# Optimization experiments

Measured on AMD Instinct MI355X. Metric: run time of the kernel, lower is better.

Reference implementation:

```python
import jax, jax.numpy as jnp
import numpy as np

DIM_HEAD = 64
REL_POS_DIM_HEAD = 32
SCALE = DIM_HEAD ** (-0.5)
REL_POS_SCALE = REL_POS_DIM_HEAD ** (-0.5)


def setup_inputs() -> dict:
    key = jax.random.key(0)
    k1, k2, k3, k4, k5 = jax.random.split(key, 5)
    B, H, S = 2, 16, 2048
    keys = jax.random.normal(k1, (B, H, S, DIM_HEAD), dtype=jnp.float32)
    queries = jax.random.normal(k2, (B, H, S, DIM_HEAD), dtype=jnp.float32)
    pos_key = jax.random.normal(k3, (B, H, S, REL_POS_DIM_HEAD), dtype=jnp.float32)
    pos_query = jax.random.normal(k4, (B, H, S, REL_POS_DIM_HEAD), dtype=jnp.float32)
    mask = jax.random.randint(k5, (B, S), 0, 2).astype(jnp.bool_)
    return {"keys": keys, "queries": queries, "pos_key": pos_key,
            "pos_query": pos_query, "mask": mask}


def reference(keys, queries, pos_key, pos_query, mask) -> jnp.ndarray:
    # clamp inputs to [-5, 5] as in the original module
    k = jnp.clip(keys, -5.0, 5.0)
    q = jnp.clip(queries, -5.0, 5.0)
    # content scores: [B, H, Q, K]
    dots = jnp.einsum("bhqd,bhkd->bhqk", q, k) * SCALE
    # relative-position scores
    pk = jnp.clip(pos_key, -5.0, 5.0)
    pq = jnp.clip(pos_query, -5.0, 5.0)
    dots = dots + jnp.einsum("bhqd,bhkd->bhqk", pq, pk) * REL_POS_SCALE
    # mask: True keys are not attended to; broadcast (B, K) -> (B, 1, 1, K)
    dots = jnp.where(mask[:, None, None, :], -jnp.inf, dots)
    return jax.nn.softmax(dots, axis=-1)
```

## Files before the change

### kernel.cpp

```cpp
#include <hip/hip_runtime.h>
#include <cstdint>
#include <cstddef>

#define SEQ 2048
#define TILES 16
#define FRAG_SHORTS 12288
#define FRAG_BYTES  24576
#define PSTRIDE 68

typedef __attribute__((ext_vector_type(8))) short bf16x8;
typedef __attribute__((ext_vector_type(4))) float f32x4;
typedef __attribute__((ext_vector_type(4))) short short4v;
typedef __attribute__((ext_vector_type(2))) unsigned uint2v;

__device__ __forceinline__ short f2bf(float f) {
    union { float f; unsigned u; } a; a.f = f;
    unsigned r = a.u + 0x7fffu + ((a.u >> 16) & 1u);
    return (short)(r >> 16);
}
__device__ __forceinline__ float clip5(float v) { return fminf(fmaxf(v, -5.0f), 5.0f); }
__device__ __forceinline__ float bflo2f(unsigned u) { union { unsigned u; float f; } a; a.u = u << 16; return a.f; }
__device__ __forceinline__ float bfhi2f(unsigned u) { union { unsigned u; float f; } a; a.u = u & 0xffff0000u; return a.f; }

__global__ __launch_bounds__(256)
void prep_kernel(const float* __restrict__ Kp, const float* __restrict__ PKp,
                 short* __restrict__ wsK)
{
    int id = blockIdx.x * 256 + threadIdx.x;
    int q = id % 24;
    int row = id / 24;
    int bh = row >> 11;
    int col = row & 2047;
    int tile = col >> 7;
    int st = (col >> 4) & 7;
    int l15 = col & 15;
    float4 v;
    int f, dd;
    if (q < 16) {
        v = reinterpret_cast<const float4*>(Kp)[(size_t)row * 16 + q];
        f = q >> 3;
        dd = (q & 7) * 4;
    } else {
        v = reinterpret_cast<const float4*>(PKp)[(size_t)row * 8 + (q - 16)];
        f = 2;
        dd = (q - 16) * 4;
    }
    int ll = l15 | ((dd >> 3) << 4);
    int j = dd & 7;
    short4v s4;
    s4[0] = f2bf(clip5(v.x)); s4[1] = f2bf(clip5(v.y));
    s4[2] = f2bf(clip5(v.z)); s4[3] = f2bf(clip5(v.w));
    *reinterpret_cast<short4v*>(wsK + ((size_t)bh * TILES + tile) * FRAG_SHORTS
                                + (((st * 3 + f) * 64 + ll) << 3) + j) = s4;
}

template<bool USEWS>
__global__ __launch_bounds__(512, 4)
void attn_map_kernel(const float* __restrict__ Kp, const float* __restrict__ Qp,
                     const float* __restrict__ PKp, const float* __restrict__ PQp,
                     const int* __restrict__ maskp, const short* __restrict__ wsK,
                     float* __restrict__ out)
{
    __shared__ short lds_k[2][FRAG_SHORTS];
    __shared__ float lds_madd[SEQ];
    __shared__ short lds_p[8 * 16 * PSTRIDE];
    __shared__ float lds_inv[128];

    const int p = blockIdx.x;
    const int x = p & 7;
    const int slot = p >> 3;
    const int bh = x + 8 * (slot >> 4);
    const int qg = slot & 15;

    const int tid = threadIdx.x;
    const int lane = tid & 63;
    const int w = tid >> 6;
    const int l15 = lane & 15;
    const int l4 = lane >> 4;

    const int qrow = qg * 128 + w * 16 + l15;

    const float* Qb  = Qp  + (size_t)bh * (SEQ * 64);
    const float* PQb = PQp + (size_t)bh * (SEQ * 32);
    const int*   mb  = maskp + (size_t)(bh >> 4) * SEQ;
    float* outb = out + (size_t)bh * SEQ * SEQ;

    const float QS  = 0.125f * 1.4426950408889634f;
    const float PQS = 0.17677669529663687f * 1.4426950408889634f;
    const float SHIFT = 28.853900817779268f;

    bf16x8 qa[3];
    #pragma unroll
    for (int f = 0; f < 2; ++f) {
        const float* src = Qb + (size_t)qrow * 64 + f * 32 + l4 * 8;
        bf16x8 v;
        #pragma unroll
        for (int j = 0; j < 8; ++j) v[j] = f2bf(clip5(src[j]) * QS);
        qa[f] = v;
    }
    {
        const float* src = PQb + (size_t)qrow * 32 + l4 * 8;
        bf16x8 v;
        #pragma unroll
        for (int j = 0; j < 8; ++j) v[j] = f2bf(clip5(src[j]) * PQS);
        qa[2] = v;
    }

    #pragma unroll
    for (int i = 0; i < SEQ / 512; ++i) {
        int idx = i * 512 + tid;
        lds_madd[idx] = (mb[idx] ? -1e30f : 0.0f) - SHIFT;
    }

    const short* kf = USEWS ? (wsK + (size_t)bh * (TILES * FRAG_SHORTS)) : nullptr;

#define STAGE(T, B) do {                                                                   \
    if constexpr (USEWS) {                                                                 \
        const char* ksrc = (const char*)kf + (size_t)(T) * FRAG_BYTES;                     \
        _Pragma("unroll")                                                                  \
        for (int c = 0; c < 3; ++c) {                                                      \
            int off = w * 3072 + c * 1024;                                                 \
            __builtin_amdgcn_global_load_lds(                                              \
                (const __attribute__((address_space(1))) void*)(ksrc + off + lane * 16),   \
                (__attribute__((address_space(3))) void*)((char*)&lds_k[(B)][0] + off),    \
                16, 0, 0);                                                                 \
        }                                                                                  \
    } else {                                                                               \
        const int tile0 = (T) * 128;                                                       \
        _Pragma("unroll")                                                                  \
        for (int i = 0; i < 6; ++i) {                                                      \
            int e = i * 512 + tid;                                                         \
            int col = e / 24, dq = e - col * 24, d0 = dq * 4;                               \
            int colg = tile0 + col;                                                        \
            float4 v; int f, dd;                                                           \
            if (d0 < 64) {                                                                 \
                v = *reinterpret_cast<const float4*>(Kp + (size_t)bh * (SEQ * 64) + (size_t)colg * 64 + d0); \
                f = d0 >> 5; dd = d0 & 31;                                                 \
            } else {                                                                       \
                v = *reinterpret_cast<const float4*>(PKp + (size_t)bh * (SEQ * 32) + (size_t)colg * 32 + (d0 - 64)); \
                f = 2; dd = d0 - 64;                                                       \
            }                                                                              \
            int ll = (col & 15) | ((dd >> 3) << 4);                                        \
            int st2 = col >> 4, j = dd & 7;                                                \
            short4v s4;                                                                    \
            s4[0] = f2bf(clip5(v.x)); s4[1] = f2bf(clip5(v.y));                            \
            s4[2] = f2bf(clip5(v.z)); s4[3] = f2bf(clip5(v.w));                            \
            *reinterpret_cast<short4v*>(&lds_k[(B)][(((st2 * 3 + f) * 64 + ll) << 3) + j]) = s4; \
        }                                                                                  \
    }                                                                                      \
} while (0)

    float ssum = 0.0f;

    STAGE(0, 0);
    __syncthreads();

    #pragma unroll 1
    for (int t = 0; t < TILES; ++t) {
        STAGE((t + 1) & 15, (t + 1) & 1);
        const short* lk = &lds_k[t & 1][0];
        #pragma unroll
        for (int st = 0; st < 8; ++st) {
            bf16x8 kb0 = *reinterpret_cast<const bf16x8*>(lk + ((st * 3 + 0) * 64 + lane) * 8);
            bf16x8 kb1 = *reinterpret_cast<const bf16x8*>(lk + ((st * 3 + 1) * 64 + lane) * 8);
            bf16x8 kb2 = *reinterpret_cast<const bf16x8*>(lk + ((st * 3 + 2) * 64 + lane) * 8);
            f32x4 madd4 = *reinterpret_cast<const f32x4*>(&lds_madd[t * 128 + st * 16 + l4 * 4]);
            f32x4 acc = {0.f, 0.f, 0.f, 0.f};
            acc = __builtin_amdgcn_mfma_f32_16x16x32_bf16(kb0, qa[0], acc, 0, 0, 0);
            acc = __builtin_amdgcn_mfma_f32_16x16x32_bf16(kb1, qa[1], acc, 0, 0, 0);
            acc = __builtin_amdgcn_mfma_f32_16x16x32_bf16(kb2, qa[2], acc, 0, 0, 0);
            float e0 = exp2f(acc[0] + madd4[0]);
            float e1 = exp2f(acc[1] + madd4[1]);
            float e2 = exp2f(acc[2] + madd4[2]);
            float e3 = exp2f(acc[3] + madd4[3]);
            ssum += (e0 + e1) + (e2 + e3);
        }
        __syncthreads();
    }

    {
        float s = ssum;
        s += __shfl_xor(s, 16);
        s += __shfl_xor(s, 32);
        if (lane < 16) lds_inv[w * 16 + l15] = 1.0f / s;
    }

    short* pw = &lds_p[w * (16 * PSTRIDE)];
    const int rowbase = qg * 128 + w * 16;

    #pragma unroll 1
    for (int t = 0; t < TILES; ++t) {
        if (t + 1 < TILES) STAGE(t + 1, (t + 1) & 1);
        const short* lk = &lds_k[t & 1][0];
        #pragma unroll
        for (int h = 0; h < 2; ++h) {
            #pragma unroll
            for (int sti = 0; sti < 4; ++sti) {
                const int st = h * 4 + sti;
                bf16x8 kb0 = *reinterpret_cast<const bf16x8*>(lk + ((st * 3 + 0) * 64 + lane) * 8);
                bf16x8 kb1 = *reinterpret_cast<const bf16x8*>(lk + ((st * 3 + 1) * 64 + lane) * 8);
                bf16x8 kb2 = *reinterpret_cast<const bf16x8*>(lk + ((st * 3 + 2) * 64 + lane) * 8);
                f32x4 madd4 = *reinterpret_cast<const f32x4*>(&lds_madd[t * 128 + st * 16 + l4 * 4]);
                f32x4 acc = {0.f, 0.f, 0.f, 0.f};
                acc = __builtin_amdgcn_mfma_f32_16x16x32_bf16(kb0, qa[0], acc, 0, 0, 0);
                acc = __builtin_amdgcn_mfma_f32_16x16x32_bf16(kb1, qa[1], acc, 0, 0, 0);
                acc = __builtin_amdgcn_mfma_f32_16x16x32_bf16(kb2, qa[2], acc, 0, 0, 0);
                float e0 = exp2f(acc[0] + madd4[0]);
                float e1 = exp2f(acc[1] + madd4[1]);
                float e2 = exp2f(acc[2] + madd4[2]);
                float e3 = exp2f(acc[3] + madd4[3]);
                unsigned u0, u1;
                asm("v_cvt_pk_bf16_f32 %0, %1, %2" : "=v"(u0) : "v"(e0), "v"(e1));
                asm("v_cvt_pk_bf16_f32 %0, %1, %2" : "=v"(u1) : "v"(e2), "v"(e3));
                uint2v uu; uu[0] = u0; uu[1] = u1;
                *reinterpret_cast<uint2v*>(&pw[l15 * PSTRIDE + sti * 16 + l4 * 4]) = uu;
            }
            #pragma unroll
            for (int s = 0; s < 4; ++s) {
                const int rl = s * 4 + (lane >> 4);
                uint2v uu = *reinterpret_cast<const uint2v*>(&pw[rl * PSTRIDE + l15 * 4]);
                const float invr = lds_inv[w * 16 + rl];
                f32x4 pv = { bflo2f(uu[0]) * invr, bfhi2f(uu[0]) * invr,
                             bflo2f(uu[1]) * invr, bfhi2f(uu[1]) * invr };
                __builtin_nontemporal_store(pv,
                    reinterpret_cast<f32x4*>(outb + (size_t)(rowbase + rl) * SEQ
                                             + t * 128 + h * 64 + l15 * 4));
            }
        }
        __syncthreads();
    }
#undef STAGE
}

extern "C" void kernel_launch(void* const* d_in, const int* in_sizes, int n_in,
                              void* d_out, int out_size, void* d_ws, size_t ws_size,
                              hipStream_t stream) {
    const float* keys      = (const float*)d_in[0];
    const float* queries   = (const float*)d_in[1];
    const float* pos_key   = (const float*)d_in[2];
    const float* pos_query = (const float*)d_in[3];
    const int*   mask      = (const int*)d_in[4];
    float* outp = (float*)d_out;

    const size_t need = (size_t)32 * TILES * FRAG_SHORTS * sizeof(short);
    if (ws_size >= need) {
        short* wsK = (short*)d_ws;
        prep_kernel<<<dim3(6144), dim3(256), 0, stream>>>(keys, pos_key, wsK);
        attn_map_kernel<true><<<dim3(512), dim3(512), 0, stream>>>(
            keys, queries, pos_key, pos_query, mask, wsK, outp);
    } else {
        attn_map_kernel<false><<<dim3(512), dim3(512), 0, stream>>>(
            keys, queries, pos_key, pos_query, mask, nullptr, outp);
    }
}
```

Before: 165.5 us.

## Split softmax row-sum pass and store pass into separate kernels

Splits the fused two-pass kernel into a sums kernel, which computes each query row's inverse softmax denominator into workspace, and a store kernel, which reads those values and writes the normalized output. The store kernel no longer carries the first pass, so its register and LDS footprint is smaller and the write-heavy phase runs on its own. This adds a kernel launch and a small global round-trip for the inverses, and recomputes the Q fragments and mask in both kernels. Output stores also switch from nontemporal to regular stores, which changes caching behaviour for the 512 MB output write.

After: 184.8 us. +11.7%, slower.

```diff
diff --git a/kernel.cpp b/kernel.cpp
--- a/kernel.cpp
+++ b/kernel.cpp
@@ -7,6 +7,8 @@
 #define FRAG_SHORTS 12288
 #define FRAG_BYTES  24576
 #define PSTRIDE 68
+#define WSK_SHORTS ((size_t)32 * TILES * FRAG_SHORTS)
+#define WSINV_FLOATS 65536
 
 typedef __attribute__((ext_vector_type(8))) short bf16x8;
 typedef __attribute__((ext_vector_type(4))) float f32x4;
@@ -21,6 +23,10 @@
 __device__ __forceinline__ float clip5(float v) { return fminf(fmaxf(v, -5.0f), 5.0f); }
 __device__ __forceinline__ float bflo2f(unsigned u) { union { unsigned u; float f; } a; a.u = u << 16; return a.f; }
 __device__ __forceinline__ float bfhi2f(unsigned u) { union { unsigned u; float f; } a; a.u = u & 0xffff0000u; return a.f; }
+
+#define QS_C  (0.125f * 1.4426950408889634f)
+#define PQS_C (0.17677669529663687f * 1.4426950408889634f)
+#define SHIFT_C 28.853900817779268f
 
 __global__ __launch_bounds__(256)
 void prep_kernel(const float* __restrict__ Kp, const float* __restrict__ PKp,
@@ -53,66 +59,6 @@
     *reinterpret_cast<short4v*>(wsK + ((size_t)bh * TILES + tile) * FRAG_SHORTS
                                 + (((st * 3 + f) * 64 + ll) << 3) + j) = s4;
 }
-
-template<bool USEWS>
-__global__ __launch_bounds__(512, 4)
-void attn_map_kernel(const float* __restrict__ Kp, const float* __restrict__ Qp,
-                     const float* __restrict__ PKp, const float* __restrict__ PQp,
-                     const int* __restrict__ maskp, const short* __restrict__ wsK,
-                     float* __restrict__ out)
-{
-    __shared__ short lds_k[2][FRAG_SHORTS];
-    __shared__ float lds_madd[SEQ];
-    __shared__ short lds_p[8 * 16 * PSTRIDE];
-    __shared__ float lds_inv[128];
-
-    const int p = blockIdx.x;
-    const int x = p & 7;
-    const int slot = p >> 3;
-    const int bh = x + 8 * (slot >> 4);
-    const int qg = slot & 15;
-
-    const int tid = threadIdx.x;
-    const int lane = tid & 63;
-    const int w = tid >> 6;
-    const int l15 = lane & 15;
-    const int l4 = lane >> 4;
-
-    const int qrow = qg * 128 + w * 16 + l15;
-
-    const float* Qb  = Qp  + (size_t)bh * (SEQ * 64);
-    const float* PQb = PQp + (size_t)bh * (SEQ * 32);
-    const int*   mb  = maskp + (size_t)(bh >> 4) * SEQ;
-    float* outb = out + (size_t)bh * SEQ * SEQ;
-
-    const float QS  = 0.125f * 1.4426950408889634f;
-    const float PQS = 0.17677669529663687f * 1.4426950408889634f;
-    const float SHIFT = 28.853900817779268f;
-
-    bf16x8 qa[3];
-    #pragma unroll
-    for (int f = 0; f < 2; ++f) {
-        const float* src = Qb + (size_t)qrow * 64 + f * 32 + l4 * 8;
-        bf16x8 v;
-        #pragma unroll
-        for (int j = 0; j < 8; ++j) v[j] = f2bf(clip5(src[j]) * QS);
-        qa[f] = v;
-    }
-    {
-        const float* src = PQb + (size_t)qrow * 32 + l4 * 8;
-        bf16x8 v;
-        #pragma unroll
-        for (int j = 0; j < 8; ++j) v[j] = f2bf(clip5(src[j]) * PQS);
-        qa[2] = v;
-    }
-
-    #pragma unroll
-    for (int i = 0; i < SEQ / 512; ++i) {
-        int idx = i * 512 + tid;
-        lds_madd[idx] = (mb[idx] ? -1e30f : 0.0f) - SHIFT;
-    }
-
-    const short* kf = USEWS ? (wsK + (size_t)bh * (TILES * FRAG_SHORTS)) : nullptr;
 
 #define STAGE(T, B) do {                                                                   \
     if constexpr (USEWS) {                                                                 \
@@ -150,14 +96,67 @@
     }                                                                                      \
 } while (0)
 
+#define PROLOGUE()                                                                          \
+    bf16x8 qa[3];                                                                           \
+    _Pragma("unroll")                                                                       \
+    for (int f = 0; f < 2; ++f) {                                                           \
+        const float* src = Qb + (size_t)qrow * 64 + f * 32 + l4 * 8;                        \
+        bf16x8 v;                                                                           \
+        _Pragma("unroll")                                                                   \
+        for (int j = 0; j < 8; ++j) v[j] = f2bf(clip5(src[j]) * QS_C);                      \
+        qa[f] = v;                                                                          \
+    }                                                                                       \
+    {                                                                                       \
+        const float* src = PQb + (size_t)qrow * 32 + l4 * 8;                                \
+        bf16x8 v;                                                                           \
+        _Pragma("unroll")                                                                   \
+        for (int j = 0; j < 8; ++j) v[j] = f2bf(clip5(src[j]) * PQS_C);                     \
+        qa[2] = v;                                                                          \
+    }                                                                                       \
+    _Pragma("unroll")                                                                       \
+    for (int i = 0; i < SEQ / 512; ++i) {                                                   \
+        int idx = i * 512 + tid;                                                            \
+        lds_madd[idx] = (mb[idx] ? -1e30f : 0.0f) - SHIFT_C;                                \
+    }
+
+template<bool USEWS>
+__global__ __launch_bounds__(512, 4)
+void sums_kernel(const float* __restrict__ Kp, const float* __restrict__ Qp,
+                 const float* __restrict__ PKp, const float* __restrict__ PQp,
+                 const int* __restrict__ maskp, const short* __restrict__ wsK,
+                 float* __restrict__ wsInv)
+{
+    __shared__ short lds_k[2][FRAG_SHORTS];
+    __shared__ float lds_madd[SEQ];
+
+    const int p = blockIdx.x;
+    const int x = p & 7;
+    const int slot = p >> 3;
+    const int bh = x + 8 * (slot >> 4);
+    const int qg = slot & 15;
+
+    const int tid = threadIdx.x;
+    const int lane = tid & 63;
+    const int w = tid >> 6;
+    const int l15 = lane & 15;
+    const int l4 = lane >> 4;
+    const int qrow = qg * 128 + w * 16 + l15;
+
+    const float* Qb  = Qp  + (size_t)bh * (SEQ * 64);
+    const float* PQb = PQp + (size_t)bh * (SEQ * 32);
+    const int*   mb  = maskp + (size_t)(bh >> 4) * SEQ;
+
+    PROLOGUE();
+
+    const short* kf = USEWS ? (wsK + (size_t)bh * (TILES * FRAG_SHORTS)) : nullptr;
+
     float ssum = 0.0f;
-
     STAGE(0, 0);
     __syncthreads();
 
     #pragma unroll 1
     for (int t = 0; t < TILES; ++t) {
-        STAGE((t + 1) & 15, (t + 1) & 1);
+        if (t + 1 < TILES) STAGE(t + 1, (t + 1) & 1);
         const short* lk = &lds_k[t & 1][0];
         #pragma unroll
         for (int st = 0; st < 8; ++st) {
@@ -178,7 +177,78 @@
         __syncthreads();
     }
 
-    {
+    float s = ssum;
+    s += __shfl_xor(s, 16);
+    s += __shfl_xor(s, 32);
+    if (lane < 16)
+        wsInv[(size_t)bh * SEQ + qrow] = 1.0f / s;
+}
+
+template<bool USEWS, bool HAVEINV>
+__global__ __launch_bounds__(512, 4)
+void store_kernel(const float* __restrict__ Kp, const float* __restrict__ Qp,
+                  const float* __restrict__ PKp, const float* __restrict__ PQp,
+                  const int* __restrict__ maskp, const short* __restrict__ wsK,
+                  const float* __restrict__ wsInv, float* __restrict__ out)
+{
+    __shared__ short lds_k[2][FRAG_SHORTS];
+    __shared__ float lds_madd[SEQ];
+    __shared__ short lds_p[8 * 16 * PSTRIDE];
+    __shared__ float lds_inv[128];
+
+    const int p = blockIdx.x;
+    const int x = p & 7;
+    const int slot = p >> 3;
+    const int bh = x + 8 * (slot >> 4);
+    const int qg = slot & 15;
+
+    const int tid = threadIdx.x;
+    const int lane = tid & 63;
+    const int w = tid >> 6;
+    const int l15 = lane & 15;
+    const int l4 = lane >> 4;
+    const int qrow = qg * 128 + w * 16 + l15;
+
+    const float* Qb  = Qp  + (size_t)bh * (SEQ * 64);
+    const float* PQb = PQp + (size_t)bh * (SEQ * 32);
+    const int*   mb  = maskp + (size_t)(bh >> 4) * SEQ;
+    float* outb = out + (size_t)bh * SEQ * SEQ;
+
+    PROLOGUE();
+
+    const short* kf = USEWS ? (wsK + (size_t)bh * (TILES * FRAG_SHORTS)) : nullptr;
+
+    STAGE(0, 0);
+
+    if constexpr (HAVEINV) {
+        if (lane < 16)
+            lds_inv[w * 16 + l15] = wsInv[(size_t)bh * SEQ + qrow];
+        __syncthreads();
+    } else {
+        __syncthreads();
+        float ssum = 0.0f;
+        #pragma unroll 1
+        for (int t = 0; t < TILES; ++t) {
+            STAGE((t + 1) & 15, (t + 1) & 1);
+            const short* lk = &lds_k[t & 1][0];
+            #pragma unroll
+            for (int st = 0; st < 8; ++st) {
+                bf16x8 kb0 = *reinterpret_cast<const bf16x8*>(lk + ((st * 3 + 0) * 64 + lane) * 8);
+                bf16x8 kb1 = *reinterpret_cast<const bf16x8*>(lk + ((st * 3 + 1) * 64 + lane) * 8);
+                bf16x8 kb2 = *reinterpret_cast<const bf16x8*>(lk + ((st * 3 + 2) * 64 + lane) * 8);
+                f32x4 madd4 = *reinterpret_cast<const f32x4*>(&lds_madd[t * 128 + st * 16 + l4 * 4]);
+                f32x4 acc = {0.f, 0.f, 0.f, 0.f};
+                acc = __builtin_amdgcn_mfma_f32_16x16x32_bf16(kb0, qa[0], acc, 0, 0, 0);
+                acc = __builtin_amdgcn_mfma_f32_16x16x32_bf16(kb1, qa[1], acc, 0, 0, 0);
+                acc = __builtin_amdgcn_mfma_f32_16x16x32_bf16(kb2, qa[2], acc, 0, 0, 0);
+                float e0 = exp2f(acc[0] + madd4[0]);
+                float e1 = exp2f(acc[1] + madd4[1]);
+                float e2 = exp2f(acc[2] + madd4[2]);
+                float e3 = exp2f(acc[3] + madd4[3]);
+                ssum += (e0 + e1) + (e2 + e3);
+            }
+            __syncthreads();
+        }
         float s = ssum;
         s += __shfl_xor(s, 16);
         s += __shfl_xor(s, 32);
@@ -222,14 +292,12 @@
                 const float invr = lds_inv[w * 16 + rl];
                 f32x4 pv = { bflo2f(uu[0]) * invr, bfhi2f(uu[0]) * invr,
                              bflo2f(uu[1]) * invr, bfhi2f(uu[1]) * invr };
-                __builtin_nontemporal_store(pv,
-                    reinterpret_cast<f32x4*>(outb + (size_t)(rowbase + rl) * SEQ
-                                             + t * 128 + h * 64 + l15 * 4));
+                *reinterpret_cast<f32x4*>(outb + (size_t)(rowbase + rl) * SEQ
+                                          + t * 128 + h * 64 + l15 * 4) = pv;
             }
         }
         __syncthreads();
     }
-#undef STAGE
 }
 
 extern "C" void kernel_launch(void* const* d_in, const int* in_sizes, int n_in,
@@ -242,14 +310,25 @@
     const int*   mask      = (const int*)d_in[4];
     float* outp = (float*)d_out;
 
-    const size_t need = (size_t)32 * TILES * FRAG_SHORTS * sizeof(short);
-    if (ws_size >= need) {
+    const size_t need_full = WSK_SHORTS * sizeof(short) + WSINV_FLOATS * sizeof(float);
+    const size_t need_inv  = WSINV_FLOATS * sizeof(float);
+
+    if (ws_size >= need_full) {
         short* wsK = (short*)d_ws;
+        float* wsInv = (float*)((char*)d_ws + WSK_SHORTS * sizeof(short));
         prep_kernel<<<dim3(6144), dim3(256), 0, stream>>>(keys, pos_key, wsK);
-        attn_map_kernel<true><<<dim3(512), dim3(512), 0, stream>>>(
-            keys, queries, pos_key, pos_query, mask, wsK, outp);
+        sums_kernel<true><<<dim3(512), dim3(512), 0, stream>>>(
+            keys, queries, pos_key, pos_query, mask, wsK, wsInv);
+        store_kernel<true, true><<<dim3(512), dim3(512), 0, stream>>>(
+            keys, queries, pos_key, pos_query, mask, wsK, wsInv, outp);
+    } else if (ws_size >= need_inv) {
+        float* wsInv = (float*)d_ws;
+        sums_kernel<false><<<dim3(512), dim3(512), 0, stream>>>(
+            keys, queries, pos_key, pos_query, mask, nullptr, wsInv);
+        store_kernel<false, true><<<dim3(512), dim3(512), 0, stream>>>(
+            keys, queries, pos_key, pos_query, mask, nullptr, wsInv, outp);
     } else {
-        attn_map_kernel<false><<<dim3(512), dim3(512), 0, stream>>>(
-            keys, queries, pos_key, pos_query, mask, nullptr, outp);
-    }
-}
+        store_kernel<false, false><<<dim3(512), dim3(512), 0, stream>>>(
+            keys, queries, pos_key, pos_query, mask, nullptr, nullptr, outp);
+    }
+}
```

## Cache exp values in registers to skip recompute; split blocks across column slices

Applied to the files above, without the earlier changes.

Each block now handles 32 query rows instead of 128. The 8 waves split into 2 row groups × 4 column slices, and the grid grows fourfold. The first pass stores the packed bf16 exponentials in a 64-entry register array. The second pass only normalizes and writes them out, with no second K staging and no MFMA recompute. Row sums are reduced across waves through shared memory. The risk is much higher VGPR pressure, which may cut occupancy or spill, and K is reloaded by four times as many blocks.

Result: faster. 149.4 us (median of 2 runs) (-9.7%).

```diff
diff --git a/kernel.cpp b/kernel.cpp
--- a/kernel.cpp
+++ b/kernel.cpp
@@ -6,7 +6,7 @@
 #define TILES 16
 #define FRAG_SHORTS 12288
 #define FRAG_BYTES  24576
-#define PSTRIDE 68
+#define PSTRIDE 36
 
 typedef __attribute__((ext_vector_type(8))) short bf16x8;
 typedef __attribute__((ext_vector_type(4))) float f32x4;
@@ -63,22 +63,25 @@
 {
     __shared__ short lds_k[2][FRAG_SHORTS];
     __shared__ float lds_madd[SEQ];
-    __shared__ short lds_p[8 * 16 * PSTRIDE];
-    __shared__ float lds_inv[128];
+    __shared__ short lds_p[8][16 * PSTRIDE];
+    __shared__ float sred[8][16];
+    __shared__ float lds_inv[8][16];
 
     const int p = blockIdx.x;
     const int x = p & 7;
     const int slot = p >> 3;
-    const int bh = x + 8 * (slot >> 4);
-    const int qg = slot & 15;
+    const int bh = x + 8 * (slot >> 6);
+    const int qb = slot & 63;
 
     const int tid = threadIdx.x;
     const int lane = tid & 63;
     const int w = tid >> 6;
     const int l15 = lane & 15;
     const int l4 = lane >> 4;
-
-    const int qrow = qg * 128 + w * 16 + l15;
+    const int rg = w & 1;
+    const int cs = w >> 1;
+
+    const int qrow = qb * 32 + rg * 16 + l15;
 
     const float* Qb  = Qp  + (size_t)bh * (SEQ * 64);
     const float* PQb = PQp + (size_t)bh * (SEQ * 32);
@@ -150,17 +153,19 @@
     }                                                                                      \
 } while (0)
 
+    unsigned pk[64];
     float ssum = 0.0f;
 
     STAGE(0, 0);
     __syncthreads();
 
-    #pragma unroll 1
+    #pragma unroll
     for (int t = 0; t < TILES; ++t) {
-        STAGE((t + 1) & 15, (t + 1) & 1);
+        if (t + 1 < TILES) STAGE(t + 1, (t + 1) & 1);
         const short* lk = &lds_k[t & 1][0];
         #pragma unroll
-        for (int st = 0; st < 8; ++st) {
+        for (int sti = 0; sti < 2; ++sti) {
+            const int st = cs * 2 + sti;
             bf16x8 kb0 = *reinterpret_cast<const bf16x8*>(lk + ((st * 3 + 0) * 64 + lane) * 8);
             bf16x8 kb1 = *reinterpret_cast<const bf16x8*>(lk + ((st * 3 + 1) * 64 + lane) * 8);
             bf16x8 kb2 = *reinterpret_cast<const bf16x8*>(lk + ((st * 3 + 2) * 64 + lane) * 8);
@@ -174,6 +179,11 @@
             float e2 = exp2f(acc[2] + madd4[2]);
             float e3 = exp2f(acc[3] + madd4[3]);
             ssum += (e0 + e1) + (e2 + e3);
+            unsigned u0, u1;
+            asm("v_cvt_pk_bf16_f32 %0, %1, %2" : "=v"(u0) : "v"(e0), "v"(e1));
+            asm("v_cvt_pk_bf16_f32 %0, %1, %2" : "=v"(u1) : "v"(e2), "v"(e3));
+            pk[t * 4 + sti * 2]     = u0;
+            pk[t * 4 + sti * 2 + 1] = u1;
         }
         __syncthreads();
     }
@@ -182,52 +192,41 @@
         float s = ssum;
         s += __shfl_xor(s, 16);
         s += __shfl_xor(s, 32);
-        if (lane < 16) lds_inv[w * 16 + l15] = 1.0f / s;
-    }
-
-    short* pw = &lds_p[w * (16 * PSTRIDE)];
-    const int rowbase = qg * 128 + w * 16;
-
-    #pragma unroll 1
+        if (lane < 16) sred[w][l15] = s;
+    }
+    __syncthreads();
+    {
+        const float rs = (sred[rg][l15] + sred[rg + 2][l15])
+                       + (sred[rg + 4][l15] + sred[rg + 6][l15]);
+        if (lane < 16) lds_inv[w][l15] = 1.0f / rs;
+    }
+
+    short* pw = &lds_p[w][0];
+    const int rowbase = qb * 32 + rg * 16;
+    const int colbase = cs * 32;
+    const int rl = lane >> 3;
+    const int cg = lane & 7;
+
+    #pragma unroll
     for (int t = 0; t < TILES; ++t) {
-        if (t + 1 < TILES) STAGE(t + 1, (t + 1) & 1);
-        const short* lk = &lds_k[t & 1][0];
-        #pragma unroll
-        for (int h = 0; h < 2; ++h) {
-            #pragma unroll
-            for (int sti = 0; sti < 4; ++sti) {
-                const int st = h * 4 + sti;
-                bf16x8 kb0 = *reinterpret_cast<const bf16x8*>(lk + ((st * 3 + 0) * 64 + lane) * 8);
-                bf16x8 kb1 = *reinterpret_cast<const bf16x8*>(lk + ((st * 3 + 1) * 64 + lane) * 8);
-                bf16x8 kb2 = *reinterpret_cast<const bf16x8*>(lk + ((st * 3 + 2) * 64 + lane) * 8);
-                f32x4 madd4 = *reinterpret_cast<const f32x4*>(&lds_madd[t * 128 + st * 16 + l4 * 4]);
-                f32x4 acc = {0.f, 0.f, 0.f, 0.f};
-                acc = __builtin_amdgcn_mfma_f32_16x16x32_bf16(kb0, qa[0], acc, 0, 0, 0);
-                acc = __builtin_amdgcn_mfma_f32_16x16x32_bf16(kb1, qa[1], acc, 0, 0, 0);
-                acc = __builtin_amdgcn_mfma_f32_16x16x32_bf16(kb2, qa[2], acc, 0, 0, 0);
-                float e0 = exp2f(acc[0] + madd4[0]);
-                float e1 = exp2f(acc[1] + madd4[1]);
-                float e2 = exp2f(acc[2] + madd4[2]);
-                float e3 = exp2f(acc[3] + madd4[3]);
-                unsigned u0, u1;
-                asm("v_cvt_pk_bf16_f32 %0, %1, %2" : "=v"(u0) : "v"(e0), "v"(e1));
-                asm("v_cvt_pk_bf16_f32 %0, %1, %2" : "=v"(u1) : "v"(e2), "v"(e3));
-                uint2v uu; uu[0] = u0; uu[1] = u1;
-                *reinterpret_cast<uint2v*>(&pw[l15 * PSTRIDE + sti * 16 + l4 * 4]) = uu;
-            }
-            #pragma unroll
-            for (int s = 0; s < 4; ++s) {
-                const int rl = s * 4 + (lane >> 4);
-                uint2v uu = *reinterpret_cast<const uint2v*>(&pw[rl * PSTRIDE + l15 * 4]);
-                const float invr = lds_inv[w * 16 + rl];
-                f32x4 pv = { bflo2f(uu[0]) * invr, bfhi2f(uu[0]) * invr,
-                             bflo2f(uu[1]) * invr, bfhi2f(uu[1]) * invr };
-                __builtin_nontemporal_store(pv,
-                    reinterpret_cast<f32x4*>(outb + (size_t)(rowbase + rl) * SEQ
-                                             + t * 128 + h * 64 + l15 * 4));
-            }
+        #pragma unroll
+        for (int sti = 0; sti < 2; ++sti) {
+            uint2v uu;
+            uu[0] = pk[t * 4 + sti * 2];
+            uu[1] = pk[t * 4 + sti * 2 + 1];
+            *reinterpret_cast<uint2v*>(&pw[l15 * PSTRIDE + sti * 16 + l4 * 4]) = uu;
         }
-        __syncthreads();
+        #pragma unroll
+        for (int sblk = 0; sblk < 2; ++sblk) {
+            const int row = sblk * 8 + rl;
+            uint2v uu = *reinterpret_cast<const uint2v*>(&pw[row * PSTRIDE + cg * 4]);
+            const float invr = lds_inv[w][row];
+            f32x4 pv = { bflo2f(uu[0]) * invr, bfhi2f(uu[0]) * invr,
+                         bflo2f(uu[1]) * invr, bfhi2f(uu[1]) * invr };
+            __builtin_nontemporal_store(pv,
+                reinterpret_cast<f32x4*>(outb + (size_t)(rowbase + row) * SEQ
+                                         + t * 128 + colbase + cg * 4));
+        }
     }
 #undef STAGE
 }
@@ -246,10 +245,10 @@
     if (ws_size >= need) {
         short* wsK = (short*)d_ws;
         prep_kernel<<<dim3(6144), dim3(256), 0, stream>>>(keys, pos_key, wsK);
-        attn_map_kernel<true><<<dim3(512), dim3(512), 0, stream>>>(
+        attn_map_kernel<true><<<dim3(2048), dim3(512), 0, stream>>>(
             keys, queries, pos_key, pos_query, mask, wsK, outp);
     } else {
-        attn_map_kernel<false><<<dim3(512), dim3(512), 0, stream>>>(
+        attn_map_kernel<false><<<dim3(2048), dim3(512), 0, stream>>>(
             keys, queries, pos_key, pos_query, mask, nullptr, outp);
     }
 }
```
